# Optimization experiments

Measured on AMD Instinct MI355X. Metric: run time of the kernel, lower is better.

Reference implementation:

```python
import jax, jax.numpy as jnp
import numpy as np

M_SIZE = 128          # local window half-size
SCALING = 1.0 / np.sqrt(64.0)


def _window_allowed(seq_len, m):
    """Boolean [L, L] mask; True where attention is allowed.

    Matches torch window_mask: window width = 2m+1; rows near the edges are
    clamped so every row sees exactly `2m+1` columns.
    """
    size = 2 * m + 1
    if seq_len <= size:
        return jnp.ones((seq_len, seq_len), dtype=bool)
    rows = jnp.arange(seq_len)[:, None]            # [L,1]
    cols = jnp.arange(seq_len)[None, :]            # [1,L]
    start = jnp.clip(rows - m, 0, seq_len - size)  # [L,1]
    return (cols >= start) & (cols < start + size)


def setup_inputs() -> dict:
    key = jax.random.key(0)
    kq, kk, kv = jax.random.split(key, 3)
    B, L, D = 8, 4096, 64
    q = jax.random.normal(kq, (B, L, D), dtype=jnp.float32)
    k = jax.random.normal(kk, (B, L, D), dtype=jnp.float32)
    v = jax.random.normal(kv, (B, L, D), dtype=jnp.float32)
    return {"q": q, "k": k, "v": v}


def reference(q, k, v):
    # scores: [B, Lq, Lk]
    scores = jnp.einsum("bqd,bkd->bqk", q, k) * SCALING
    allowed = _window_allowed(q.shape[1], M_SIZE)          # [L, L]
    scores = jnp.where(allowed[None, :, :], scores, -jnp.inf)
    attention = jax.nn.softmax(scores, axis=2)
    out = jnp.einsum("bqk,bkv->bqv", attention, v)
    return (out, attention)
```

## Files before the change

kernel.cpp:

```cpp
#include <hip/hip_runtime.h>
#include <math.h>

#define L_SEQ 4096
#define D_HEAD 64
#define M_WIN 128
#define WIN 257
#define QB 8
#define W 264
#define WF4 66
#define ATTS 272
#define SCALE 0.125f

#define RL(v, i) __uint_as_float(__builtin_amdgcn_readlane(__float_as_uint(v), (i)))

static __device__ __forceinline__ unsigned bfr(float x) {
    unsigned u = __float_as_uint(x);
    return (u + 0x7fffu + ((u >> 16) & 1u)) >> 16;
}
static __device__ __forceinline__ unsigned bfpack(float lo, float hi) {
    return bfr(lo) | (bfr(hi) << 16);
}
static __device__ __forceinline__ float bf2f(unsigned h) {
    return __uint_as_float(h << 16);
}

__global__ __launch_bounds__(256, 4) void win_attn_kernel(
    const float* __restrict__ Q, const float* __restrict__ K,
    const float* __restrict__ V, float* __restrict__ OutO,
    float* __restrict__ OutA)
{
    extern __shared__ float smem[];
    uint4*  k_su  = (uint4*)smem;
    unsigned short* att_h = (unsigned short*)(smem + 2112 * 4);

    const int t  = threadIdx.x;
    const int w  = t >> 6;
    const int ln = t & 63;
    const int bid = blockIdx.x;
    const int b   = bid >> 9;
    const int q0  = (bid & 511) * QB;

    int s0 = q0 - M_WIN;
    if (s0 < 0) s0 = 0;
    if (s0 > L_SEQ - WIN) s0 = L_SEQ - WIN;
    const int wcount = (L_SEQ - s0 < W) ? (L_SEQ - s0) : W;

    {
        const float4* Kg = (const float4*)(K + ((size_t)(b * L_SEQ + s0)) * D_HEAD);
        #pragma unroll 3
        for (int idx = t; idx < 264 * 8; idx += 256) {
            int row = idx >> 3, c8 = idx & 7;
            int gr  = (row < wcount) ? row : wcount - 1;
            float4 a  = Kg[(size_t)gr * 16 + c8 * 2];
            float4 bb = Kg[(size_t)gr * 16 + c8 * 2 + 1];
            uint4 d;
            d.x = bfpack(a.x, a.y);   d.y = bfpack(a.z, a.w);
            d.z = bfpack(bb.x, bb.y); d.w = bfpack(bb.z, bb.w);
            k_su[row * 8 + (c8 ^ (row & 7))] = d;
        }
    }
    const int r0g = q0 + 2 * w;
    const float qv0 = Q[((size_t)(b * L_SEQ) + r0g)     * D_HEAD + ln];
    const float qv1 = Q[((size_t)(b * L_SEQ) + r0g + 1) * D_HEAD + ln];
    if (ln < 16) {
        int r = 2 * w + (ln >> 3);
        att_h[r * ATTS + 264 + (ln & 7)] = 0;
    }
    __syncthreads();

    float p0[5], p1[5];
    {
        const uint4* kp[5];
        int msk[5];
        #pragma unroll
        for (int cg = 0; cg < 5; ++cg) {
            int colr = cg * 64 + ln;
            int col  = (colr < W) ? colr : W - 1;
            kp[cg]  = k_su + (size_t)col * 8;
            msk[cg] = col & 7;
            p0[cg] = 0.f; p1[cg] = 0.f;
        }
        #pragma unroll
        for (int c8 = 0; c8 < 8; ++c8) {
            float a0 = RL(qv0, 8*c8+0), a1 = RL(qv0, 8*c8+1),
                  a2 = RL(qv0, 8*c8+2), a3 = RL(qv0, 8*c8+3),
                  a4 = RL(qv0, 8*c8+4), a5 = RL(qv0, 8*c8+5),
                  a6 = RL(qv0, 8*c8+6), a7 = RL(qv0, 8*c8+7);
            float b0 = RL(qv1, 8*c8+0), b1 = RL(qv1, 8*c8+1),
                  b2 = RL(qv1, 8*c8+2), b3 = RL(qv1, 8*c8+3),
                  b4 = RL(qv1, 8*c8+4), b5 = RL(qv1, 8*c8+5),
                  b6 = RL(qv1, 8*c8+6), b7 = RL(qv1, 8*c8+7);
            #pragma unroll
            for (int cg = 0; cg < 5; ++cg) {
                uint4 kk = kp[cg][c8 ^ msk[cg]];
                float e0 = __uint_as_float(kk.x << 16);
                float e1 = __uint_as_float(kk.x & 0xffff0000u);
                float e2 = __uint_as_float(kk.y << 16);
                float e3 = __uint_as_float(kk.y & 0xffff0000u);
                float e4 = __uint_as_float(kk.z << 16);
                float e5 = __uint_as_float(kk.z & 0xffff0000u);
                float e6 = __uint_as_float(kk.w << 16);
                float e7 = __uint_as_float(kk.w & 0xffff0000u);
                p0[cg] += a0*e0 + a1*e1 + a2*e2 + a3*e3
                        + a4*e4 + a5*e5 + a6*e6 + a7*e7;
                p1[cg] += b0*e0 + b1*e1 + b2*e2 + b3*e3
                        + b4*e4 + b5*e5 + b6*e6 + b7*e7;
            }
        }
        #pragma unroll
        for (int cg = 0; cg < 5; ++cg) { p0[cg] *= SCALE; p1[cg] *= SCALE; }
    }

    {
        int st0 = r0g - M_WIN;
        if (st0 < 0) st0 = 0;
        if (st0 > L_SEQ - WIN) st0 = L_SEQ - WIN;
        const int lo0 = st0 - s0;
        int st1 = r0g + 1 - M_WIN;
        if (st1 < 0) st1 = 0;
        if (st1 > L_SEQ - WIN) st1 = L_SEQ - WIN;
        const int lo1 = st1 - s0;

        float m0 = -1e30f, m1 = -1e30f;
        #pragma unroll
        for (int cg = 0; cg < 5; ++cg) {
            int colr = cg * 64 + ln;
            bool in0 = (colr >= lo0) && (colr < lo0 + WIN);
            bool in1 = (colr >= lo1) && (colr < lo1 + WIN);
            p0[cg] = in0 ? p0[cg] : -1e30f;
            p1[cg] = in1 ? p1[cg] : -1e30f;
            m0 = fmaxf(m0, p0[cg]);
            m1 = fmaxf(m1, p1[cg]);
        }
        #pragma unroll
        for (int off = 32; off >= 1; off >>= 1) {
            m0 = fmaxf(m0, __shfl_xor(m0, off));
            m1 = fmaxf(m1, __shfl_xor(m1, off));
        }
        float sum0 = 0.f, sum1 = 0.f;
        #pragma unroll
        for (int cg = 0; cg < 5; ++cg) {
            float e0 = (p0[cg] <= -1e29f) ? 0.f : __expf(p0[cg] - m0);
            float e1 = (p1[cg] <= -1e29f) ? 0.f : __expf(p1[cg] - m1);
            p0[cg] = e0; p1[cg] = e1;
            sum0 += e0; sum1 += e1;
        }
        #pragma unroll
        for (int off = 32; off >= 1; off >>= 1) {
            sum0 += __shfl_xor(sum0, off);
            sum1 += __shfl_xor(sum1, off);
        }
        const float inv0 = 1.f / sum0, inv1 = 1.f / sum1;
        #pragma unroll
        for (int cg = 0; cg < 5; ++cg) {
            int colr = cg * 64 + ln;
            if (colr < W) {
                att_h[(2 * w)     * ATTS + colr] = (unsigned short)bfr(p0[cg] * inv0);
                att_h[(2 * w + 1) * ATTS + colr] = (unsigned short)bfr(p1[cg] * inv1);
            }
        }
    }

    {
        const int cq = ln >> 4;
        const int dg = ln & 15;
        const float4* Vg4 = (const float4*)(V + ((size_t)(b * L_SEQ + s0)) * D_HEAD);
        const uint2* a2r0 = (const uint2*)(att_h + (2 * w) * ATTS);
        const uint2* a2r1 = (const uint2*)(att_h + (2 * w + 1) * ATTS);
        float4 acc0 = {0.f,0.f,0.f,0.f}, acc1 = {0.f,0.f,0.f,0.f};
        #pragma unroll 2
        for (int G = 0; G < 17; ++G) {
            uint2 ua = a2r0[4 * G + cq];
            uint2 ub = a2r1[4 * G + cq];
            float pa[4], pb[4];
            pa[0] = bf2f(ua.x & 0xffffu); pa[1] = bf2f(ua.x >> 16);
            pa[2] = bf2f(ua.y & 0xffffu); pa[3] = bf2f(ua.y >> 16);
            pb[0] = bf2f(ub.x & 0xffffu); pb[1] = bf2f(ub.x >> 16);
            pb[2] = bf2f(ub.y & 0xffffu); pb[3] = bf2f(ub.y >> 16);
            #pragma unroll
            for (int e = 0; e < 4; ++e) {
                int col  = 16 * G + 4 * cq + e;
                int colc = (col < wcount) ? col : wcount - 1;
                float4 vv = Vg4[(size_t)colc * 16 + dg];
                float fa = pa[e], fb = pb[e];
                acc0.x += fa * vv.x; acc0.y += fa * vv.y;
                acc0.z += fa * vv.z; acc0.w += fa * vv.w;
                acc1.x += fb * vv.x; acc1.y += fb * vv.y;
                acc1.z += fb * vv.z; acc1.w += fb * vv.w;
            }
        }
        #pragma unroll
        for (int off = 16; off <= 32; off <<= 1) {
            acc0.x += __shfl_xor(acc0.x, off); acc0.y += __shfl_xor(acc0.y, off);
            acc0.z += __shfl_xor(acc0.z, off); acc0.w += __shfl_xor(acc0.w, off);
            acc1.x += __shfl_xor(acc1.x, off); acc1.y += __shfl_xor(acc1.y, off);
            acc1.z += __shfl_xor(acc1.z, off); acc1.w += __shfl_xor(acc1.w, off);
        }
        if (ln < 16) {
            float4* o4 = (float4*)(OutO + ((size_t)(b * L_SEQ + r0g)) * D_HEAD);
            o4[dg]      = acc0;
            o4[16 + dg] = acc1;
        }
    }

    if ((s0 & 3) == 0) {
        const int zlo = s0 >> 2;
        #pragma unroll
        for (int r = 0; r < 2; ++r) {
            float4* rowp = (float4*)(OutA + ((size_t)(b * L_SEQ + r0g + r)) * L_SEQ);
            const uint2* arow = (const uint2*)(att_h + (2 * w + r) * ATTS);
            #pragma unroll 4
            for (int j = 0; j < 16; ++j) {
                int f4i = j * 64 + ln;
                int u4  = f4i - zlo;
                float4 wv = {0.f,0.f,0.f,0.f};
                if (u4 >= 0 && u4 < WF4) {
                    uint2 uu = arow[u4];
                    wv.x = bf2f(uu.x & 0xffffu); wv.y = bf2f(uu.x >> 16);
                    wv.z = bf2f(uu.y & 0xffffu); wv.w = bf2f(uu.y >> 16);
                }
                rowp[f4i] = wv;
            }
        }
    } else {
        #pragma unroll
        for (int r = 0; r < 2; ++r) {
            float4* rowp = (float4*)(OutA + ((size_t)(b * L_SEQ + r0g + r)) * L_SEQ);
            const unsigned short* arow = att_h + (2 * w + r) * ATTS;
            #pragma unroll 2
            for (int j = 0; j < 16; ++j) {
                int f4i = j * 64 + ln;
                int u   = 4 * f4i - s0;
                float4 wv;
                wv.x = (u     >= 0 && u     < W) ? bf2f(arow[u])     : 0.f;
                wv.y = (u + 1 >= 0 && u + 1 < W) ? bf2f(arow[u + 1]) : 0.f;
                wv.z = (u + 2 >= 0 && u + 2 < W) ? bf2f(arow[u + 2]) : 0.f;
                wv.w = (u + 3 >= 0 && u + 3 < W) ? bf2f(arow[u + 3]) : 0.f;
                rowp[f4i] = wv;
            }
        }
    }
}

extern "C" void kernel_launch(void* const* d_in, const int* in_sizes, int n_in,
                              void* d_out, int out_size, void* d_ws, size_t ws_size,
                              hipStream_t stream) {
    const float* Q = (const float*)d_in[0];
    const float* K = (const float*)d_in[1];
    const float* V = (const float*)d_in[2];
    float* OutO = (float*)d_out;
    float* OutA = OutO + (size_t)8 * L_SEQ * D_HEAD;

    const int smem_bytes = 2112 * 16 + QB * ATTS * 2;
    hipFuncSetAttribute((const void*)win_attn_kernel,
                        hipFuncAttributeMaxDynamicSharedMemorySize, smem_bytes);

    dim3 grid(8 * (L_SEQ / QB));
    dim3 block(256);
    win_attn_kernel<<<grid, block, smem_bytes, stream>>>(Q, K, V, OutO, OutA);
}
```

Measured before the change: 160.9 us.

## Process two query tiles per block sharing one staged K window

```diff
diff --git a/kernel.cpp b/kernel.cpp
--- a/kernel.cpp
+++ b/kernel.cpp
@@ -6,6 +6,9 @@
 #define M_WIN 128
 #define WIN 257
 #define QB 8
+#define NT 2
+#define QBLK 16
+#define KROWS 272
 #define W 264
 #define WF4 66
 #define ATTS 272
@@ -31,212 +34,227 @@
 {
     extern __shared__ float smem[];
     uint4*  k_su  = (uint4*)smem;
-    unsigned short* att_h = (unsigned short*)(smem + 2112 * 4);
+    unsigned short* att_h = (unsigned short*)(smem + 8704);
 
     const int t  = threadIdx.x;
     const int w  = t >> 6;
     const int ln = t & 63;
     const int bid = blockIdx.x;
-    const int b   = bid >> 9;
-    const int q0  = (bid & 511) * QB;
-
-    int s0 = q0 - M_WIN;
-    if (s0 < 0) s0 = 0;
-    if (s0 > L_SEQ - WIN) s0 = L_SEQ - WIN;
-    const int wcount = (L_SEQ - s0 < W) ? (L_SEQ - s0) : W;
+    const int b      = bid >> 8;
+    const int q0_blk = (bid & 255) * QBLK;
+
+    int s0_blk = q0_blk - M_WIN;
+    if (s0_blk < 0) s0_blk = 0;
+    if (s0_blk > L_SEQ - KROWS) s0_blk = L_SEQ - KROWS;
 
     {
-        const float4* Kg = (const float4*)(K + ((size_t)(b * L_SEQ + s0)) * D_HEAD);
+        const float4* Kg = (const float4*)(K + ((size_t)(b * L_SEQ + s0_blk)) * D_HEAD);
         #pragma unroll 3
-        for (int idx = t; idx < 264 * 8; idx += 256) {
+        for (int idx = t; idx < KROWS * 8; idx += 256) {
             int row = idx >> 3, c8 = idx & 7;
-            int gr  = (row < wcount) ? row : wcount - 1;
-            float4 a  = Kg[(size_t)gr * 16 + c8 * 2];
-            float4 bb = Kg[(size_t)gr * 16 + c8 * 2 + 1];
+            float4 a  = Kg[(size_t)row * 16 + c8 * 2];
+            float4 bb = Kg[(size_t)row * 16 + c8 * 2 + 1];
             uint4 d;
             d.x = bfpack(a.x, a.y);   d.y = bfpack(a.z, a.w);
             d.z = bfpack(bb.x, bb.y); d.w = bfpack(bb.z, bb.w);
             k_su[row * 8 + (c8 ^ (row & 7))] = d;
         }
     }
-    const int r0g = q0 + 2 * w;
-    const float qv0 = Q[((size_t)(b * L_SEQ) + r0g)     * D_HEAD + ln];
-    const float qv1 = Q[((size_t)(b * L_SEQ) + r0g + 1) * D_HEAD + ln];
+    float qv[NT][2];
+    #pragma unroll
+    for (int ti = 0; ti < NT; ++ti) {
+        int rg = q0_blk + ti * QB + 2 * w;
+        qv[ti][0] = Q[((size_t)(b * L_SEQ) + rg)     * D_HEAD + ln];
+        qv[ti][1] = Q[((size_t)(b * L_SEQ) + rg + 1) * D_HEAD + ln];
+    }
     if (ln < 16) {
         int r = 2 * w + (ln >> 3);
         att_h[r * ATTS + 264 + (ln & 7)] = 0;
     }
     __syncthreads();
 
-    float p0[5], p1[5];
-    {
-        const uint4* kp[5];
-        int msk[5];
-        #pragma unroll
-        for (int cg = 0; cg < 5; ++cg) {
-            int colr = cg * 64 + ln;
-            int col  = (colr < W) ? colr : W - 1;
-            kp[cg]  = k_su + (size_t)col * 8;
-            msk[cg] = col & 7;
-            p0[cg] = 0.f; p1[cg] = 0.f;
-        }
-        #pragma unroll
-        for (int c8 = 0; c8 < 8; ++c8) {
-            float a0 = RL(qv0, 8*c8+0), a1 = RL(qv0, 8*c8+1),
-                  a2 = RL(qv0, 8*c8+2), a3 = RL(qv0, 8*c8+3),
-                  a4 = RL(qv0, 8*c8+4), a5 = RL(qv0, 8*c8+5),
-                  a6 = RL(qv0, 8*c8+6), a7 = RL(qv0, 8*c8+7);
-            float b0 = RL(qv1, 8*c8+0), b1 = RL(qv1, 8*c8+1),
-                  b2 = RL(qv1, 8*c8+2), b3 = RL(qv1, 8*c8+3),
-                  b4 = RL(qv1, 8*c8+4), b5 = RL(qv1, 8*c8+5),
-                  b6 = RL(qv1, 8*c8+6), b7 = RL(qv1, 8*c8+7);
-            #pragma unroll
-            for (int cg = 0; cg < 5; ++cg) {
-                uint4 kk = kp[cg][c8 ^ msk[cg]];
-                float e0 = __uint_as_float(kk.x << 16);
-                float e1 = __uint_as_float(kk.x & 0xffff0000u);
-                float e2 = __uint_as_float(kk.y << 16);
-                float e3 = __uint_as_float(kk.y & 0xffff0000u);
-                float e4 = __uint_as_float(kk.z << 16);
-                float e5 = __uint_as_float(kk.z & 0xffff0000u);
-                float e6 = __uint_as_float(kk.w << 16);
-                float e7 = __uint_as_float(kk.w & 0xffff0000u);
-                p0[cg] += a0*e0 + a1*e1 + a2*e2 + a3*e3
-                        + a4*e4 + a5*e5 + a6*e6 + a7*e7;
-                p1[cg] += b0*e0 + b1*e1 + b2*e2 + b3*e3
-                        + b4*e4 + b5*e5 + b6*e6 + b7*e7;
-            }
-        }
-        #pragma unroll
-        for (int cg = 0; cg < 5; ++cg) { p0[cg] *= SCALE; p1[cg] *= SCALE; }
-    }
-
-    {
-        int st0 = r0g - M_WIN;
-        if (st0 < 0) st0 = 0;
-        if (st0 > L_SEQ - WIN) st0 = L_SEQ - WIN;
-        const int lo0 = st0 - s0;
-        int st1 = r0g + 1 - M_WIN;
-        if (st1 < 0) st1 = 0;
-        if (st1 > L_SEQ - WIN) st1 = L_SEQ - WIN;
-        const int lo1 = st1 - s0;
-
-        float m0 = -1e30f, m1 = -1e30f;
-        #pragma unroll
-        for (int cg = 0; cg < 5; ++cg) {
-            int colr = cg * 64 + ln;
-            bool in0 = (colr >= lo0) && (colr < lo0 + WIN);
-            bool in1 = (colr >= lo1) && (colr < lo1 + WIN);
-            p0[cg] = in0 ? p0[cg] : -1e30f;
-            p1[cg] = in1 ? p1[cg] : -1e30f;
-            m0 = fmaxf(m0, p0[cg]);
-            m1 = fmaxf(m1, p1[cg]);
-        }
-        #pragma unroll
-        for (int off = 32; off >= 1; off >>= 1) {
-            m0 = fmaxf(m0, __shfl_xor(m0, off));
-            m1 = fmaxf(m1, __shfl_xor(m1, off));
-        }
-        float sum0 = 0.f, sum1 = 0.f;
-        #pragma unroll
-        for (int cg = 0; cg < 5; ++cg) {
-            float e0 = (p0[cg] <= -1e29f) ? 0.f : __expf(p0[cg] - m0);
-            float e1 = (p1[cg] <= -1e29f) ? 0.f : __expf(p1[cg] - m1);
-            p0[cg] = e0; p1[cg] = e1;
-            sum0 += e0; sum1 += e1;
-        }
-        #pragma unroll
-        for (int off = 32; off >= 1; off >>= 1) {
-            sum0 += __shfl_xor(sum0, off);
-            sum1 += __shfl_xor(sum1, off);
-        }
-        const float inv0 = 1.f / sum0, inv1 = 1.f / sum1;
-        #pragma unroll
-        for (int cg = 0; cg < 5; ++cg) {
-            int colr = cg * 64 + ln;
-            if (colr < W) {
-                att_h[(2 * w)     * ATTS + colr] = (unsigned short)bfr(p0[cg] * inv0);
-                att_h[(2 * w + 1) * ATTS + colr] = (unsigned short)bfr(p1[cg] * inv1);
-            }
-        }
-    }
-
-    {
-        const int cq = ln >> 4;
-        const int dg = ln & 15;
-        const float4* Vg4 = (const float4*)(V + ((size_t)(b * L_SEQ + s0)) * D_HEAD);
-        const uint2* a2r0 = (const uint2*)(att_h + (2 * w) * ATTS);
-        const uint2* a2r1 = (const uint2*)(att_h + (2 * w + 1) * ATTS);
-        float4 acc0 = {0.f,0.f,0.f,0.f}, acc1 = {0.f,0.f,0.f,0.f};
-        #pragma unroll 2
-        for (int G = 0; G < 17; ++G) {
-            uint2 ua = a2r0[4 * G + cq];
-            uint2 ub = a2r1[4 * G + cq];
-            float pa[4], pb[4];
-            pa[0] = bf2f(ua.x & 0xffffu); pa[1] = bf2f(ua.x >> 16);
-            pa[2] = bf2f(ua.y & 0xffffu); pa[3] = bf2f(ua.y >> 16);
-            pb[0] = bf2f(ub.x & 0xffffu); pb[1] = bf2f(ub.x >> 16);
-            pb[2] = bf2f(ub.y & 0xffffu); pb[3] = bf2f(ub.y >> 16);
-            #pragma unroll
-            for (int e = 0; e < 4; ++e) {
-                int col  = 16 * G + 4 * cq + e;
-                int colc = (col < wcount) ? col : wcount - 1;
-                float4 vv = Vg4[(size_t)colc * 16 + dg];
-                float fa = pa[e], fb = pb[e];
-                acc0.x += fa * vv.x; acc0.y += fa * vv.y;
-                acc0.z += fa * vv.z; acc0.w += fa * vv.w;
-                acc1.x += fb * vv.x; acc1.y += fb * vv.y;
-                acc1.z += fb * vv.z; acc1.w += fb * vv.w;
-            }
-        }
-        #pragma unroll
-        for (int off = 16; off <= 32; off <<= 1) {
-            acc0.x += __shfl_xor(acc0.x, off); acc0.y += __shfl_xor(acc0.y, off);
-            acc0.z += __shfl_xor(acc0.z, off); acc0.w += __shfl_xor(acc0.w, off);
-            acc1.x += __shfl_xor(acc1.x, off); acc1.y += __shfl_xor(acc1.y, off);
-            acc1.z += __shfl_xor(acc1.z, off); acc1.w += __shfl_xor(acc1.w, off);
-        }
-        if (ln < 16) {
-            float4* o4 = (float4*)(OutO + ((size_t)(b * L_SEQ + r0g)) * D_HEAD);
-            o4[dg]      = acc0;
-            o4[16 + dg] = acc1;
-        }
-    }
-
-    if ((s0 & 3) == 0) {
-        const int zlo = s0 >> 2;
-        #pragma unroll
-        for (int r = 0; r < 2; ++r) {
-            float4* rowp = (float4*)(OutA + ((size_t)(b * L_SEQ + r0g + r)) * L_SEQ);
-            const uint2* arow = (const uint2*)(att_h + (2 * w + r) * ATTS);
-            #pragma unroll 4
-            for (int j = 0; j < 16; ++j) {
-                int f4i = j * 64 + ln;
-                int u4  = f4i - zlo;
-                float4 wv = {0.f,0.f,0.f,0.f};
-                if (u4 >= 0 && u4 < WF4) {
-                    uint2 uu = arow[u4];
-                    wv.x = bf2f(uu.x & 0xffffu); wv.y = bf2f(uu.x >> 16);
-                    wv.z = bf2f(uu.y & 0xffffu); wv.w = bf2f(uu.y >> 16);
-                }
-                rowp[f4i] = wv;
-            }
-        }
-    } else {
-        #pragma unroll
-        for (int r = 0; r < 2; ++r) {
-            float4* rowp = (float4*)(OutA + ((size_t)(b * L_SEQ + r0g + r)) * L_SEQ);
-            const unsigned short* arow = att_h + (2 * w + r) * ATTS;
+    #pragma unroll
+    for (int ti = 0; ti < NT; ++ti) {
+        const int q0  = q0_blk + ti * QB;
+        const int r0g = q0 + 2 * w;
+        int s0 = q0 - M_WIN;
+        if (s0 < 0) s0 = 0;
+        if (s0 > L_SEQ - WIN) s0 = L_SEQ - WIN;
+        const int off    = s0 - s0_blk;
+        const int wcount = (L_SEQ - s0 < W) ? (L_SEQ - s0) : W;
+        const float qv0 = qv[ti][0], qv1 = qv[ti][1];
+
+        float p0[5], p1[5];
+        {
+            const uint4* kp[5];
+            int msk[5];
+            #pragma unroll
+            for (int cg = 0; cg < 5; ++cg) {
+                int colr = cg * 64 + ln;
+                int col  = (colr < wcount) ? colr : wcount - 1;
+                int row  = off + col;
+                kp[cg]  = k_su + (size_t)row * 8;
+                msk[cg] = row & 7;
+                p0[cg] = 0.f; p1[cg] = 0.f;
+            }
+            #pragma unroll
+            for (int c8 = 0; c8 < 8; ++c8) {
+                float a0 = RL(qv0, 8*c8+0), a1 = RL(qv0, 8*c8+1),
+                      a2 = RL(qv0, 8*c8+2), a3 = RL(qv0, 8*c8+3),
+                      a4 = RL(qv0, 8*c8+4), a5 = RL(qv0, 8*c8+5),
+                      a6 = RL(qv0, 8*c8+6), a7 = RL(qv0, 8*c8+7);
+                float b0 = RL(qv1, 8*c8+0), b1 = RL(qv1, 8*c8+1),
+                      b2 = RL(qv1, 8*c8+2), b3 = RL(qv1, 8*c8+3),
+                      b4 = RL(qv1, 8*c8+4), b5 = RL(qv1, 8*c8+5),
+                      b6 = RL(qv1, 8*c8+6), b7 = RL(qv1, 8*c8+7);
+                #pragma unroll
+                for (int cg = 0; cg < 5; ++cg) {
+                    uint4 kk = kp[cg][c8 ^ msk[cg]];
+                    float e0 = __uint_as_float(kk.x << 16);
+                    float e1 = __uint_as_float(kk.x & 0xffff0000u);
+                    float e2 = __uint_as_float(kk.y << 16);
+                    float e3 = __uint_as_float(kk.y & 0xffff0000u);
+                    float e4 = __uint_as_float(kk.z << 16);
+                    float e5 = __uint_as_float(kk.z & 0xffff0000u);
+                    float e6 = __uint_as_float(kk.w << 16);
+                    float e7 = __uint_as_float(kk.w & 0xffff0000u);
+                    p0[cg] += a0*e0 + a1*e1 + a2*e2 + a3*e3
+                            + a4*e4 + a5*e5 + a6*e6 + a7*e7;
+                    p1[cg] += b0*e0 + b1*e1 + b2*e2 + b3*e3
+                            + b4*e4 + b5*e5 + b6*e6 + b7*e7;
+                }
+            }
+            #pragma unroll
+            for (int cg = 0; cg < 5; ++cg) { p0[cg] *= SCALE; p1[cg] *= SCALE; }
+        }
+
+        {
+            int st0 = r0g - M_WIN;
+            if (st0 < 0) st0 = 0;
+            if (st0 > L_SEQ - WIN) st0 = L_SEQ - WIN;
+            const int lo0 = st0 - s0;
+            int st1 = r0g + 1 - M_WIN;
+            if (st1 < 0) st1 = 0;
+            if (st1 > L_SEQ - WIN) st1 = L_SEQ - WIN;
+            const int lo1 = st1 - s0;
+
+            float m0 = -1e30f, m1 = -1e30f;
+            #pragma unroll
+            for (int cg = 0; cg < 5; ++cg) {
+                int colr = cg * 64 + ln;
+                bool in0 = (colr >= lo0) && (colr < lo0 + WIN);
+                bool in1 = (colr >= lo1) && (colr < lo1 + WIN);
+                p0[cg] = in0 ? p0[cg] : -1e30f;
+                p1[cg] = in1 ? p1[cg] : -1e30f;
+                m0 = fmaxf(m0, p0[cg]);
+                m1 = fmaxf(m1, p1[cg]);
+            }
+            #pragma unroll
+            for (int o = 32; o >= 1; o >>= 1) {
+                m0 = fmaxf(m0, __shfl_xor(m0, o));
+                m1 = fmaxf(m1, __shfl_xor(m1, o));
+            }
+            float sum0 = 0.f, sum1 = 0.f;
+            #pragma unroll
+            for (int cg = 0; cg < 5; ++cg) {
+                float e0 = (p0[cg] <= -1e29f) ? 0.f : __expf(p0[cg] - m0);
+                float e1 = (p1[cg] <= -1e29f) ? 0.f : __expf(p1[cg] - m1);
+                p0[cg] = e0; p1[cg] = e1;
+                sum0 += e0; sum1 += e1;
+            }
+            #pragma unroll
+            for (int o = 32; o >= 1; o >>= 1) {
+                sum0 += __shfl_xor(sum0, o);
+                sum1 += __shfl_xor(sum1, o);
+            }
+            const float inv0 = 1.f / sum0, inv1 = 1.f / sum1;
+            #pragma unroll
+            for (int cg = 0; cg < 5; ++cg) {
+                int colr = cg * 64 + ln;
+                if (colr < W) {
+                    att_h[(2 * w)     * ATTS + colr] = (unsigned short)bfr(p0[cg] * inv0);
+                    att_h[(2 * w + 1) * ATTS + colr] = (unsigned short)bfr(p1[cg] * inv1);
+                }
+            }
+        }
+
+        {
+            const int cq = ln >> 4;
+            const int dg = ln & 15;
+            const float4* Vg4 = (const float4*)(V + ((size_t)(b * L_SEQ + s0)) * D_HEAD);
+            const uint2* a2r0 = (const uint2*)(att_h + (2 * w) * ATTS);
+            const uint2* a2r1 = (const uint2*)(att_h + (2 * w + 1) * ATTS);
+            float4 acc0 = {0.f,0.f,0.f,0.f}, acc1 = {0.f,0.f,0.f,0.f};
             #pragma unroll 2
-            for (int j = 0; j < 16; ++j) {
-                int f4i = j * 64 + ln;
-                int u   = 4 * f4i - s0;
-                float4 wv;
-                wv.x = (u     >= 0 && u     < W) ? bf2f(arow[u])     : 0.f;
-                wv.y = (u + 1 >= 0 && u + 1 < W) ? bf2f(arow[u + 1]) : 0.f;
-                wv.z = (u + 2 >= 0 && u + 2 < W) ? bf2f(arow[u + 2]) : 0.f;
-                wv.w = (u + 3 >= 0 && u + 3 < W) ? bf2f(arow[u + 3]) : 0.f;
-                rowp[f4i] = wv;
+            for (int G = 0; G < 17; ++G) {
+                uint2 ua = a2r0[4 * G + cq];
+                uint2 ub = a2r1[4 * G + cq];
+                float pa[4], pb[4];
+                pa[0] = bf2f(ua.x & 0xffffu); pa[1] = bf2f(ua.x >> 16);
+                pa[2] = bf2f(ua.y & 0xffffu); pa[3] = bf2f(ua.y >> 16);
+                pb[0] = bf2f(ub.x & 0xffffu); pb[1] = bf2f(ub.x >> 16);
+                pb[2] = bf2f(ub.y & 0xffffu); pb[3] = bf2f(ub.y >> 16);
+                #pragma unroll
+                for (int e = 0; e < 4; ++e) {
+                    int col  = 16 * G + 4 * cq + e;
+                    int colc = (col < wcount) ? col : wcount - 1;
+                    float4 vv = Vg4[(size_t)colc * 16 + dg];
+                    float fa = pa[e], fb = pb[e];
+                    acc0.x += fa * vv.x; acc0.y += fa * vv.y;
+                    acc0.z += fa * vv.z; acc0.w += fa * vv.w;
+                    acc1.x += fb * vv.x; acc1.y += fb * vv.y;
+                    acc1.z += fb * vv.z; acc1.w += fb * vv.w;
+                }
+            }
+            #pragma unroll
+            for (int o = 16; o <= 32; o <<= 1) {
+                acc0.x += __shfl_xor(acc0.x, o); acc0.y += __shfl_xor(acc0.y, o);
+                acc0.z += __shfl_xor(acc0.z, o); acc0.w += __shfl_xor(acc0.w, o);
+                acc1.x += __shfl_xor(acc1.x, o); acc1.y += __shfl_xor(acc1.y, o);
+                acc1.z += __shfl_xor(acc1.z, o); acc1.w += __shfl_xor(acc1.w, o);
+            }
+            if (ln < 16) {
+                float4* o4 = (float4*)(OutO + ((size_t)(b * L_SEQ + r0g)) * D_HEAD);
+                o4[dg]      = acc0;
+                o4[16 + dg] = acc1;
+            }
+        }
+
+        if ((s0 & 3) == 0) {
+            const int zlo = s0 >> 2;
+            #pragma unroll
+            for (int r = 0; r < 2; ++r) {
+                float4* rowp = (float4*)(OutA + ((size_t)(b * L_SEQ + r0g + r)) * L_SEQ);
+                const uint2* arow = (const uint2*)(att_h + (2 * w + r) * ATTS);
+                #pragma unroll 4
+                for (int j = 0; j < 16; ++j) {
+                    int f4i = j * 64 + ln;
+                    int u4  = f4i - zlo;
+                    float4 wv = {0.f,0.f,0.f,0.f};
+                    if (u4 >= 0 && u4 < WF4) {
+                        uint2 uu = arow[u4];
+                        wv.x = bf2f(uu.x & 0xffffu); wv.y = bf2f(uu.x >> 16);
+                        wv.z = bf2f(uu.y & 0xffffu); wv.w = bf2f(uu.y >> 16);
+                    }
+                    rowp[f4i] = wv;
+                }
+            }
+        } else {
+            #pragma unroll
+            for (int r = 0; r < 2; ++r) {
+                float4* rowp = (float4*)(OutA + ((size_t)(b * L_SEQ + r0g + r)) * L_SEQ);
+                const unsigned short* arow = att_h + (2 * w + r) * ATTS;
+                #pragma unroll 2
+                for (int j = 0; j < 16; ++j) {
+                    int f4i = j * 64 + ln;
+                    int u   = 4 * f4i - s0;
+                    float4 wv;
+                    wv.x = (u     >= 0 && u     < W) ? bf2f(arow[u])     : 0.f;
+                    wv.y = (u + 1 >= 0 && u + 1 < W) ? bf2f(arow[u + 1]) : 0.f;
+                    wv.z = (u + 2 >= 0 && u + 2 < W) ? bf2f(arow[u + 2]) : 0.f;
+                    wv.w = (u + 3 >= 0 && u + 3 < W) ? bf2f(arow[u + 3]) : 0.f;
+                    rowp[f4i] = wv;
+                }
             }
         }
     }
@@ -251,11 +269,11 @@
     float* OutO = (float*)d_out;
     float* OutA = OutO + (size_t)8 * L_SEQ * D_HEAD;
 
-    const int smem_bytes = 2112 * 16 + QB * ATTS * 2;
+    const int smem_bytes = KROWS * 128 + QB * ATTS * 2;
     hipFuncSetAttribute((const void*)win_attn_kernel,
                         hipFuncAttributeMaxDynamicSharedMemorySize, smem_bytes);
 
-    dim3 grid(8 * (L_SEQ / QB));
+    dim3 grid(8 * (L_SEQ / QBLK));
     dim3 block(256);
     win_attn_kernel<<<grid, block, smem_bytes, stream>>>(Q, K, V, OutO, OutA);
 }
```

After: 149.8 us. -6.9%, faster.
